# Kernel tuning notes

Measured on AMD Instinct MI355X. Metric: run time of the kernel, lower is better.

## Reference

```python
import jax, jax.numpy as jnp
import numpy as np

B = 65536
IN = 512
SEQ = 4
LN_EPS = 1e-5


def _ln(x, g, b, eps=LN_EPS):
    # LayerNorm over last dim with affine params
    m = jnp.mean(x, axis=-1, keepdims=True)
    v = jnp.mean((x - m) ** 2, axis=-1, keepdims=True)
    return (x - m) * jax.lax.rsqrt(v + eps) * g + b


def setup_inputs() -> dict:
    key = jax.random.key(0)
    ks = jax.random.split(key, 24)

    def lin(k, shape, fan_in):
        return jax.random.normal(k, shape, jnp.float32) / np.sqrt(fan_in)

    return {
        "x": jax.random.normal(ks[0], (B, IN), jnp.float32),
        "history": jax.random.normal(ks[1], (B, SEQ * IN), jnp.float32),
        # gate network: (seq*in)->64->32
        "g1_w": lin(ks[2], (64, SEQ * IN), SEQ * IN), "g1_b": lin(ks[3], (64,), SEQ * IN),
        "g2_w": lin(ks[4], (32, 64), 64), "g2_b": lin(ks[5], (32,), 64),
        # base modulated layer in->128
        "base_w": lin(ks[6], (128, IN), IN), "base_b": lin(ks[7], (128,), IN),
        "ln1_g": jnp.ones((128,), jnp.float32), "ln1_b": jnp.zeros((128,), jnp.float32),
        # main network: NoisyLinear(eval) 128->64, LN(64), Linear 64->32
        "n1_w": lin(ks[8], (64, 128), 128), "n1_b": lin(ks[9], (64,), 128),
        "ln2_g": jnp.ones((64,), jnp.float32), "ln2_b": jnp.zeros((64,), jnp.float32),
        "m_w": lin(ks[10], (32, 64), 64), "m_b": lin(ks[11], (32,), 64),
        # value stream 32->16->1
        "v1_w": lin(ks[12], (16, 32), 32), "v1_b": lin(ks[13], (16,), 32),
        "v2_w": lin(ks[14], (1, 16), 16), "v2_b": lin(ks[15], (1,), 16),
        # advantage stream 32->16->4 (NoisyLinear in eval mode = mu only)
        "a1_w": lin(ks[16], (16, 32), 32), "a1_b": lin(ks[17], (16,), 32),
        "a2_w": lin(ks[18], (4, 16), 16), "a2_b": lin(ks[19], (4,), 16),
    }


def reference(x, history, g1_w, g1_b, g2_w, g2_b, base_w, base_b, ln1_g, ln1_b,
              n1_w, n1_b, ln2_g, ln2_b, m_w, m_b,
              v1_w, v1_b, v2_w, v2_b, a1_w, a1_b, a2_w, a2_b):
    # gate network
    h = jax.nn.relu(history @ g1_w.T + g1_b)
    gate_values = jax.nn.sigmoid(h @ g2_w.T + g2_b)            # [B, 32]
    mod = 0.7 + 0.3 * jnp.mean(gate_values, axis=1, keepdims=True)  # [B, 1]

    # per-sample scalar weight modulation: bmm(x, (mod*W)^T) == (x @ W^T) * mod
    x_gated = (x @ base_w.T) * mod + base_b                    # [B, 128]
    x_gated = _ln(jax.nn.relu(x_gated), ln1_g, ln1_b)

    # main network (NoisyLinear in eval mode -> mu weights)
    f = jax.nn.relu(x_gated @ n1_w.T + n1_b)
    f = _ln(f, ln2_g, ln2_b)
    features = jax.nn.relu(f @ m_w.T + m_b)                    # [B, 32]

    value = jax.nn.relu(features @ v1_w.T + v1_b) @ v2_w.T + v2_b    # [B, 1]
    advantage = jax.nn.relu(features @ a1_w.T + a1_b) @ a2_w.T + a2_b  # [B, 4]

    q_values = value + (advantage - jnp.mean(advantage, axis=1, keepdims=True))
    return q_values, gate_values
```

## Files before the change

### kernel.cpp

```cpp
#include <hip/hip_runtime.h>
#include <hip/hip_bf16.h>

typedef float f32x4 __attribute__((ext_vector_type(4)));
typedef __bf16 bf16x8 __attribute__((ext_vector_type(8)));
typedef unsigned int u32;
typedef u32 u32x4 __attribute__((ext_vector_type(4)));

#define PK1  0
#define PK2  131072
#define PK3  133120
#define PK4  264192
#define PK5  280576
#define PK6V 284672
#define PK6A 285696

__device__ __forceinline__ f32x4 mfma16(bf16x8 a, bf16x8 b, f32x4 c) {
    return __builtin_amdgcn_mfma_f32_16x16x32_bf16(a, b, c, 0, 0, 0);
}
__device__ __forceinline__ float redsum16(float v) {
    v += __shfl_xor(v, 1); v += __shfl_xor(v, 2);
    v += __shfl_xor(v, 4); v += __shfl_xor(v, 8);
    return v;
}
__device__ __forceinline__ unsigned short bfb(__bf16 b) {
    return __builtin_bit_cast(unsigned short, b);
}
__device__ __forceinline__ f32x4 ldnt(const float* p) {
    return __builtin_nontemporal_load((const f32x4*)p);
}
__device__ __forceinline__ bf16x8 cvt8(f32x4 a, f32x4 b) {
    bf16x8 r;
    r[0]=(__bf16)a[0]; r[1]=(__bf16)a[1]; r[2]=(__bf16)a[2]; r[3]=(__bf16)a[3];
    r[4]=(__bf16)b[0]; r[5]=(__bf16)b[1]; r[6]=(__bf16)b[2]; r[7]=(__bf16)b[3];
    return r;
}
__device__ __forceinline__ void split8(f32x4 a, f32x4 b, bf16x8& h, bf16x8& l) {
    #pragma unroll
    for (int e=0;e<4;++e){ __bf16 hb=(__bf16)a[e]; h[e]=hb; l[e]=(__bf16)(a[e]-(float)hb); }
    #pragma unroll
    for (int e=0;e<4;++e){ __bf16 hb=(__bf16)b[e]; h[4+e]=hb; l[4+e]=(__bf16)(b[e]-(float)hb); }
}
__device__ __forceinline__ void unpack8(u32x4 w0, u32x4 w1, bf16x8& h, bf16x8& l) {
    u32 h0=(w0[0]&0xFFFFu)|(w0[1]<<16), h1=(w0[2]&0xFFFFu)|(w0[3]<<16);
    u32 h2=(w1[0]&0xFFFFu)|(w1[1]<<16), h3=(w1[2]&0xFFFFu)|(w1[3]<<16);
    u32 l0=(w0[0]>>16)|(w0[1]&0xFFFF0000u), l1=(w0[2]>>16)|(w0[3]&0xFFFF0000u);
    u32 l2=(w1[0]>>16)|(w1[1]&0xFFFF0000u), l3=(w1[2]>>16)|(w1[3]&0xFFFF0000u);
    u32x4 hv={h0,h1,h2,h3}, lv={l0,l1,l2,l3};
    h=__builtin_bit_cast(bf16x8,hv); l=__builtin_bit_cast(bf16x8,lv);
}

__device__ __forceinline__ void pack_plain(const float* __restrict__ W, __bf16* __restrict__ dst,
                                           int i, int K, int Nn) {
    int e=i&7, lane=(i>>3)&63, p=i>>9;
    int n=p%Nn, t=p/Nn;
    float v = W[(size_t)(n*16+(lane&15))*K + t*32 + (lane>>4)*8 + e];
    dst[i] = (__bf16)v;
}
__device__ __forceinline__ void pack_hilo(const float* __restrict__ W, __bf16* __restrict__ dst,
                                          int i, int K, int Nn) {
    int e=i&7, lane=(i>>3)&63, p=i>>9;
    int n=p%Nn, t=p/Nn;
    float v = W[(size_t)(n*16+(lane&15))*K + t*32 + (lane>>4)*8 + e];
    __bf16 h = (__bf16)v;
    dst[p*1024 + (i&511)]       = h;
    dst[p*1024 + 512 + (i&511)] = (__bf16)(v - (float)h);
}
__global__ void pack_weights(const float* g1w, const float* g2w, const float* bw,
                             const float* n1w, const float* mw, const float* v1w,
                             const float* a1w, __bf16* wsb) {
    int gi = blockIdx.x*256 + threadIdx.x;
    if      (gi < 131072) pack_plain(g1w, wsb+PK1, gi,          2048, 4);
    else if (gi < 133120) pack_plain(g2w, wsb+PK2, gi-131072,   64,   2);
    else if (gi < 198656) pack_hilo (bw,  wsb+PK3, gi-133120,   512,  8);
    else if (gi < 206848) pack_hilo (n1w, wsb+PK4, gi-198656,   128,  4);
    else if (gi < 208896) pack_hilo (mw,  wsb+PK5, gi-206848,   64,   2);
    else if (gi < 209408) pack_hilo (v1w, wsb+PK6V, gi-208896,  32,   1);
    else if (gi < 209920) pack_hilo (a1w, wsb+PK6A, gi-209408,  32,   1);
}

__global__ __launch_bounds__(256, 4)
void gated_dqn_main(const float* __restrict__ x,   const float* __restrict__ hist,
                    const float* __restrict__ g1b, const float* __restrict__ g2b,
                    const float* __restrict__ bb,  const float* __restrict__ ln1g,
                    const float* __restrict__ ln1b,const float* __restrict__ n1b,
                    const float* __restrict__ ln2g,const float* __restrict__ ln2b,
                    const float* __restrict__ mb,  const float* __restrict__ v1b,
                    const float* __restrict__ v2w, const float* __restrict__ v2b,
                    const float* __restrict__ a1b, const float* __restrict__ a2w,
                    const float* __restrict__ a2b, const __bf16* __restrict__ wsb,
                    float* __restrict__ qout, float* __restrict__ gateout)
{
    __shared__ __align__(16) float scr[4][2112];
    const int tid = threadIdx.x, lane = tid & 63, wv = tid >> 6;
    const int qq = lane >> 4, c = lane & 15;
    const int r0 = (blockIdx.x*4 + wv)*16;
    float*  myA = scr[wv];
    u32*    my  = (u32*)myA;
    __bf16* myb = (__bf16*)myA;
    const int swc = ((c >> 1) & 3) << 3;
    const int srl = lane >> 3, scl = lane & 7;

    f32x4 acc[4] = {};
    {
        const float* aRow0 = hist + (size_t)(r0 + srl)*2048 + scl*4;
        const float* aRow1 = hist + (size_t)(r0 + 8 + srl)*2048 + scl*4;
        f32x4 rg[8];
        #pragma unroll
        for (int q = 0; q < 4; ++q) {
            rg[q]   = ldnt(aRow0 + q*32);
            rg[4+q] = ldnt(aRow1 + q*32);
        }
        const __bf16* bB = wsb + PK1 + lane*8;
        bf16x8 cb0 = *(const bf16x8*)(bB),      cb1 = *(const bf16x8*)(bB+512);
        bf16x8 cb2 = *(const bf16x8*)(bB+1024), cb3 = *(const bf16x8*)(bB+1536);
        for (int g = 0; g < 16; ++g) {
            #pragma unroll
            for (int q = 0; q < 4; ++q) {
                *(f32x4*)&myA[srl*132     + q*32 + scl*4] = rg[q];
                *(f32x4*)&myA[(8+srl)*132 + q*32 + scl*4] = rg[4+q];
            }
            if (g + 1 < 16) {
                #pragma unroll
                for (int q = 0; q < 4; ++q) {
                    rg[q]   = ldnt(aRow0 + (g+1)*128 + q*32);
                    rg[4+q] = ldnt(aRow1 + (g+1)*128 + q*32);
                }
            }
            #pragma unroll
            for (int t = 0; t < 4; ++t) {
                int ktn = g*4 + t + 1; if (ktn > 63) ktn = 63;
                const __bf16* btn = bB + (size_t)ktn*2048;
                bf16x8 nb0 = *(const bf16x8*)(btn),      nb1 = *(const bf16x8*)(btn+512);
                bf16x8 nb2 = *(const bf16x8*)(btn+1024), nb3 = *(const bf16x8*)(btn+1536);
                f32x4 lo = *(const f32x4*)&myA[c*132 + t*32 + qq*8];
                f32x4 hi = *(const f32x4*)&myA[c*132 + t*32 + qq*8 + 4];
                bf16x8 af = cvt8(lo, hi);
                acc[0] = mfma16(af, cb0, acc[0]); acc[1] = mfma16(af, cb1, acc[1]);
                acc[2] = mfma16(af, cb2, acc[2]); acc[3] = mfma16(af, cb3, acc[3]);
                cb0 = nb0; cb1 = nb1; cb2 = nb2; cb3 = nb3;
            }
        }
        #pragma unroll
        for (int n = 0; n < 4; ++n) {
            float bv = g1b[n*16 + c];
            #pragma unroll
            for (int j = 0; j < 4; ++j) {
                int r = qq*4 + j, col = n*16 + c;
                myb[r*64 + (col ^ (((r>>1)&3)<<3))] = (__bf16)fmaxf(acc[n][j] + bv, 0.0f);
            }
        }
    }

    float mj[4];
    {
        const __bf16* bB = wsb + PK2 + lane*8;
        bf16x8 a0 = *(const bf16x8*)&myb[c*64 + ((qq*8) ^ swc)];
        bf16x8 a1 = *(const bf16x8*)&myb[c*64 + ((32 + qq*8) ^ swc)];
        bf16x8 b00 = *(const bf16x8*)(bB),      b01 = *(const bf16x8*)(bB+512);
        bf16x8 b10 = *(const bf16x8*)(bB+1024), b11 = *(const bf16x8*)(bB+1536);
        f32x4 ag0 = {}, ag1 = {};
        ag0 = mfma16(a0, b00, ag0); ag1 = mfma16(a0, b01, ag1);
        ag0 = mfma16(a1, b10, ag0); ag1 = mfma16(a1, b11, ag1);
        float s[4] = {0,0,0,0};
        #pragma unroll
        for (int n = 0; n < 2; ++n) {
            float bv = g2b[n*16 + c];
            f32x4 ag = n ? ag1 : ag0;
            #pragma unroll
            for (int j = 0; j < 4; ++j) {
                float gv = 1.0f / (1.0f + __expf(-(ag[j] + bv)));
                __builtin_nontemporal_store(gv,
                    gateout + (size_t)(r0 + qq*4 + j)*32 + n*16 + c);
                s[j] += gv;
            }
        }
        #pragma unroll
        for (int j = 0; j < 4; ++j)
            mj[j] = 0.7f + 0.3f * redsum16(s[j]) * (1.0f/32.0f);
    }

    f32x4 a3[8] = {};
    {
        const float* aRow0 = x + (size_t)(r0 + srl)*512 + scl*4;
        const float* aRow1 = x + (size_t)(r0 + 8 + srl)*512 + scl*4;
        f32x4 rg[8];
        #pragma unroll
        for (int q = 0; q < 4; ++q) {
            rg[q]   = ldnt(aRow0 + q*32);
            rg[4+q] = ldnt(aRow1 + q*32);
        }
        for (int g = 0; g < 4; ++g) {
            #pragma unroll
            for (int q = 0; q < 4; ++q) {
                *(f32x4*)&myA[srl*132     + q*32 + scl*4] = rg[q];
                *(f32x4*)&myA[(8+srl)*132 + q*32 + scl*4] = rg[4+q];
            }
            if (g + 1 < 4) {
                #pragma unroll
                for (int q = 0; q < 4; ++q) {
                    rg[q]   = ldnt(aRow0 + (g+1)*128 + q*32);
                    rg[4+q] = ldnt(aRow1 + (g+1)*128 + q*32);
                }
            }
            #pragma unroll
            for (int t = 0; t < 4; ++t) {
                f32x4 lo = *(const f32x4*)&myA[c*132 + t*32 + qq*8];
                f32x4 hi = *(const f32x4*)&myA[c*132 + t*32 + qq*8 + 4];
                bf16x8 ah, al; split8(lo, hi, ah, al);
                int kt = g*4 + t;
                #pragma unroll
                for (int half = 0; half < 2; ++half) {
                    const __bf16* bt = wsb + PK3 + (size_t)(kt*16 + half*8)*512 + lane*8;
                    #pragma unroll
                    for (int n = 0; n < 4; ++n) {
                        bf16x8 bh = *(const bf16x8*)(bt + n*1024);
                        f32x4 a = a3[half*4 + n];
                        a = mfma16(ah, bh, a); a = mfma16(al, bh, a);
                        a3[half*4 + n] = a;
                    }
                }
            }
        }
        float s[4] = {0,0,0,0}, ss[4] = {0,0,0,0};
        #pragma unroll
        for (int n = 0; n < 8; ++n) {
            float bv = bb[n*16 + c];
            #pragma unroll
            for (int j = 0; j < 4; ++j) {
                float v = fmaxf(a3[n][j]*mj[j] + bv, 0.0f);
                a3[n][j] = v; s[j] += v; ss[j] += v*v;
            }
        }
        float mean[4], rstd[4];
        #pragma unroll
        for (int j = 0; j < 4; ++j) {
            float t = redsum16(s[j]), t2 = redsum16(ss[j]);
            float m = t * (1.0f/128.0f);
            mean[j] = m; rstd[j] = rsqrtf(t2*(1.0f/128.0f) - m*m + 1e-5f);
        }
        #pragma unroll
        for (int n = 0; n < 8; ++n) {
            float g = ln1g[n*16 + c], b2 = ln1b[n*16 + c];
            #pragma unroll
            for (int j = 0; j < 4; ++j) {
                int r = qq*4 + j, col = n*16 + c;
                float y = (a3[n][j] - mean[j]) * rstd[j] * g + b2;
                __bf16 hb = (__bf16)y; __bf16 lb = (__bf16)(y - (float)hb);
                my[r*128 + (col ^ (((r>>1)&3)<<3))] = (u32)bfb(hb) | ((u32)bfb(lb) << 16);
            }
        }
    }

    f32x4 a4[4] = {};
    {
        const __bf16* bB = wsb + PK4 + lane*8;
        #pragma unroll
        for (int t = 0; t < 4; ++t) {
            int base = c*128 + ((t*32 + qq*8) ^ swc);
            u32x4 w0 = *(const u32x4*)&my[base], w1 = *(const u32x4*)&my[base + 4];
            bf16x8 ah, al; unpack8(w0, w1, ah, al);
            const __bf16* bt = bB + t*4096;
            #pragma unroll
            for (int n = 0; n < 4; ++n) {
                bf16x8 bh = *(const bf16x8*)(bt + n*1024);
                f32x4 a = a4[n];
                a = mfma16(ah, bh, a); a = mfma16(al, bh, a);
                a4[n] = a;
            }
        }
        float s[4] = {0,0,0,0}, ss[4] = {0,0,0,0};
        #pragma unroll
        for (int n = 0; n < 4; ++n) {
            float bv = n1b[n*16 + c];
            #pragma unroll
            for (int j = 0; j < 4; ++j) {
                float v = fmaxf(a4[n][j] + bv, 0.0f);
                a4[n][j] = v; s[j] += v; ss[j] += v*v;
            }
        }
        float mean[4], rstd[4];
        #pragma unroll
        for (int j = 0; j < 4; ++j) {
            float t = redsum16(s[j]), t2 = redsum16(ss[j]);
            float m = t * (1.0f/64.0f);
            mean[j] = m; rstd[j] = rsqrtf(t2*(1.0f/64.0f) - m*m + 1e-5f);
        }
        #pragma unroll
        for (int n = 0; n < 4; ++n) {
            float g = ln2g[n*16 + c], b2 = ln2b[n*16 + c];
            #pragma unroll
            for (int j = 0; j < 4; ++j) {
                int r = qq*4 + j, col = n*16 + c;
                float y = (a4[n][j] - mean[j]) * rstd[j] * g + b2;
                __bf16 hb = (__bf16)y; __bf16 lb = (__bf16)(y - (float)hb);
                my[r*64 + (col ^ (((r>>1)&3)<<3))] = (u32)bfb(hb) | ((u32)bfb(lb) << 16);
            }
        }
    }

    {
        const __bf16* bB = wsb + PK5 + lane*8;
        f32x4 a5[2] = {};
        #pragma unroll
        for (int t = 0; t < 2; ++t) {
            int base = c*64 + ((t*32 + qq*8) ^ swc);
            u32x4 w0 = *(const u32x4*)&my[base], w1 = *(const u32x4*)&my[base + 4];
            bf16x8 ah, al; unpack8(w0, w1, ah, al);
            const __bf16* bt = bB + t*2048;
            #pragma unroll
            for (int n = 0; n < 2; ++n) {
                bf16x8 bh = *(const bf16x8*)(bt + n*1024);
                f32x4 a = a5[n];
                a = mfma16(ah, bh, a); a = mfma16(al, bh, a);
                a5[n] = a;
            }
        }
        #pragma unroll
        for (int n = 0; n < 2; ++n) {
            float bv = mb[n*16 + c];
            #pragma unroll
            for (int j = 0; j < 4; ++j) {
                int r = qq*4 + j, col = n*16 + c;
                float v = fmaxf(a5[n][j] + bv, 0.0f);
                __bf16 hb = (__bf16)v; __bf16 lb = (__bf16)(v - (float)hb);
                my[r*32 + (col ^ (((r>>1)&3)<<3))] = (u32)bfb(hb) | ((u32)bfb(lb) << 16);
            }
        }
    }

    {
        int base = c*32 + ((qq*8) ^ swc);
        u32x4 w0 = *(const u32x4*)&my[base], w1 = *(const u32x4*)&my[base + 4];
        bf16x8 ah, al; unpack8(w0, w1, ah, al);
        const __bf16* bv_ = wsb + PK6V + lane*8;
        const __bf16* ba_ = wsb + PK6A + lane*8;
        bf16x8 vh  = *(const bf16x8*)(bv_);
        bf16x8 ahw = *(const bf16x8*)(ba_);
        f32x4 av = {}, aa = {};
        av = mfma16(ah, vh, av);  av = mfma16(al, vh, av);
        aa = mfma16(ah, ahw, aa); aa = mfma16(al, ahw, aa);
        float v1bc = v1b[c], a1bc = a1b[c], w2 = v2w[c];
        float vb2 = v2b[0];
        float aw0 = a2w[c], aw1 = a2w[16+c], aw2 = a2w[32+c], aw3 = a2w[48+c];
        float ab0 = a2b[0], ab1 = a2b[1], ab2 = a2b[2], ab3 = a2b[3];
        #pragma unroll
        for (int j = 0; j < 4; ++j) {
            float hv = fmaxf(av[j] + v1bc, 0.0f);
            float ha = fmaxf(aa[j] + a1bc, 0.0f);
            float val = redsum16(hv * w2) + vb2;
            float d0 = redsum16(ha * aw0) + ab0;
            float d1 = redsum16(ha * aw1) + ab1;
            float d2 = redsum16(ha * aw2) + ab2;
            float d3 = redsum16(ha * aw3) + ab3;
            float ma = 0.25f * (d0 + d1 + d2 + d3);
            if (c == 0) {
                f32x4 qv = {val + d0 - ma, val + d1 - ma, val + d2 - ma, val + d3 - ma};
                __builtin_nontemporal_store(qv,
                    (f32x4*)(qout + (size_t)(r0 + qq*4 + j)*4));
            }
        }
    }
}

extern "C" void kernel_launch(void* const* d_in, const int* in_sizes, int n_in,
                              void* d_out, int out_size, void* d_ws, size_t ws_size,
                              hipStream_t stream) {
    (void)in_sizes; (void)n_in; (void)ws_size; (void)out_size;
    const float* x    = (const float*)d_in[0];
    const float* hist = (const float*)d_in[1];
    const float* g1w  = (const float*)d_in[2];
    const float* g1b  = (const float*)d_in[3];
    const float* g2w  = (const float*)d_in[4];
    const float* g2b  = (const float*)d_in[5];
    const float* bw   = (const float*)d_in[6];
    const float* bb   = (const float*)d_in[7];
    const float* ln1g = (const float*)d_in[8];
    const float* ln1b = (const float*)d_in[9];
    const float* n1w  = (const float*)d_in[10];
    const float* n1b  = (const float*)d_in[11];
    const float* ln2g = (const float*)d_in[12];
    const float* ln2b = (const float*)d_in[13];
    const float* mw   = (const float*)d_in[14];
    const float* mb   = (const float*)d_in[15];
    const float* v1w  = (const float*)d_in[16];
    const float* v1b  = (const float*)d_in[17];
    const float* v2w  = (const float*)d_in[18];
    const float* v2b  = (const float*)d_in[19];
    const float* a1w  = (const float*)d_in[20];
    const float* a1b  = (const float*)d_in[21];
    const float* a2w  = (const float*)d_in[22];
    const float* a2b  = (const float*)d_in[23];
    __bf16* wsb = (__bf16*)d_ws;
    float* qout = (float*)d_out;
    float* gateout = qout + (size_t)65536 * 4;

    pack_weights<<<dim3(820), dim3(256), 0, stream>>>(g1w, g2w, bw, n1w, mw, v1w, a1w, wsb);
    gated_dqn_main<<<dim3(1024), dim3(256), 0, stream>>>(
        x, hist, g1b, g2b, bb, ln1g, ln1b, n1b, ln2g, ln2b, mb,
        v1b, v2w, v2b, a1b, a2w, a2b, wsb, qout, gateout);
}
```

Baseline: 164.7 us.

## Deepen prefetch pipeline in gate GEMM with double-buffered history and weight registers

Restructures the history×g1_w loop so two history chunks are in flight at once (prefetch distance of two groups instead of one). It also loads a whole group's 16 weight fragments ahead into a ping-pong register set, replacing the per-k-step fetch. The loop is fully unrolled, and launch bounds drop from 4 to 2 blocks per CU to make room for the extra registers. The aim is to hide more global memory latency on this bandwidth-bound stream, at the cost of lower occupancy.

```diff
diff --git a/kernel.cpp b/kernel.cpp
--- a/kernel.cpp
+++ b/kernel.cpp
@@ -78,7 +78,7 @@
     else if (gi < 209920) pack_hilo (a1w, wsb+PK6A, gi-209408,  32,   1);
 }
 
-__global__ __launch_bounds__(256, 4)
+__global__ __launch_bounds__(256, 2)
 void gated_dqn_main(const float* __restrict__ x,   const float* __restrict__ hist,
                     const float* __restrict__ g1b, const float* __restrict__ g2b,
                     const float* __restrict__ bb,  const float* __restrict__ ln1g,
@@ -104,41 +104,53 @@
     {
         const float* aRow0 = hist + (size_t)(r0 + srl)*2048 + scl*4;
         const float* aRow1 = hist + (size_t)(r0 + 8 + srl)*2048 + scl*4;
-        f32x4 rg[8];
+        const __bf16* bB = wsb + PK1 + lane*8;
+        f32x4 rgA[8], rgB[8];
+        bf16x8 Bc[16], Bn[16];
+        #pragma unroll
+        for (int i = 0; i < 16; ++i) Bc[i] = *(const bf16x8*)(bB + (size_t)i*512);
         #pragma unroll
         for (int q = 0; q < 4; ++q) {
-            rg[q]   = ldnt(aRow0 + q*32);
-            rg[4+q] = ldnt(aRow1 + q*32);
-        }
-        const __bf16* bB = wsb + PK1 + lane*8;
-        bf16x8 cb0 = *(const bf16x8*)(bB),      cb1 = *(const bf16x8*)(bB+512);
-        bf16x8 cb2 = *(const bf16x8*)(bB+1024), cb3 = *(const bf16x8*)(bB+1536);
-        for (int g = 0; g < 16; ++g) {
+            rgA[q]   = ldnt(aRow0 + q*32);
+            rgA[4+q] = ldnt(aRow1 + q*32);
+        }
+        #pragma unroll
+        for (int q = 0; q < 4; ++q) {
+            rgB[q]   = ldnt(aRow0 + 128 + q*32);
+            rgB[4+q] = ldnt(aRow1 + 128 + q*32);
+        }
+        auto body = [&](int g, f32x4* rgS, bf16x8* BcL, bf16x8* BnL) {
             #pragma unroll
             for (int q = 0; q < 4; ++q) {
-                *(f32x4*)&myA[srl*132     + q*32 + scl*4] = rg[q];
-                *(f32x4*)&myA[(8+srl)*132 + q*32 + scl*4] = rg[4+q];
+                *(f32x4*)&myA[srl*132     + q*32 + scl*4] = rgS[q];
+                *(f32x4*)&myA[(8+srl)*132 + q*32 + scl*4] = rgS[4+q];
             }
             if (g + 1 < 16) {
                 #pragma unroll
+                for (int i = 0; i < 16; ++i)
+                    BnL[i] = *(const bf16x8*)(bB + (size_t)(g+1)*8192 + i*512);
+            }
+            if (g + 2 < 16) {
+                #pragma unroll
                 for (int q = 0; q < 4; ++q) {
-                    rg[q]   = ldnt(aRow0 + (g+1)*128 + q*32);
-                    rg[4+q] = ldnt(aRow1 + (g+1)*128 + q*32);
+                    rgS[q]   = ldnt(aRow0 + (g+2)*128 + q*32);
+                    rgS[4+q] = ldnt(aRow1 + (g+2)*128 + q*32);
                 }
             }
             #pragma unroll
             for (int t = 0; t < 4; ++t) {
-                int ktn = g*4 + t + 1; if (ktn > 63) ktn = 63;
-                const __bf16* btn = bB + (size_t)ktn*2048;
-                bf16x8 nb0 = *(const bf16x8*)(btn),      nb1 = *(const bf16x8*)(btn+512);
-                bf16x8 nb2 = *(const bf16x8*)(btn+1024), nb3 = *(const bf16x8*)(btn+1536);
                 f32x4 lo = *(const f32x4*)&myA[c*132 + t*32 + qq*8];
                 f32x4 hi = *(const f32x4*)&myA[c*132 + t*32 + qq*8 + 4];
                 bf16x8 af = cvt8(lo, hi);
-                acc[0] = mfma16(af, cb0, acc[0]); acc[1] = mfma16(af, cb1, acc[1]);
-                acc[2] = mfma16(af, cb2, acc[2]); acc[3] = mfma16(af, cb3, acc[3]);
-                cb0 = nb0; cb1 = nb1; cb2 = nb2; cb3 = nb3;
-            }
+                #pragma unroll
+                for (int n = 0; n < 4; ++n)
+                    acc[n] = mfma16(af, BcL[t*4 + n], acc[n]);
+            }
+        };
+        #pragma unroll
+        for (int gp = 0; gp < 8; ++gp) {
+            body(2*gp,     rgA, Bc, Bn);
+            body(2*gp + 1, rgB, Bn, Bc);
         }
         #pragma unroll
         for (int n = 0; n < 4; ++n) {
```

New measurement: 161.2 us. 2.1% less time.
